# Performance work log

Measured on AMD Instinct MI355X. Metric: run time of the kernel, lower is better.

Reference implementation:

```python
import jax, jax.numpy as jnp
import numpy as np

H, D = 4, 32            # heads, head_dim
HID = H * D             # hidden_channels = 128
L = 2                   # num_layers
N = (100000, 50000)     # (n_session, n_item)
E = 200000              # edges per relation
ETYPES = ((0, 1), (1, 0), (1, 1))  # (src_type, dst_type) per relation


def _seg_softmax(alpha, dst, num_dst):
    # alpha: [E, H]; softmax over edges sharing the same dst node
    amax = jax.ops.segment_max(alpha, dst, num_segments=num_dst)
    amax = jnp.where(jnp.isfinite(amax), amax, 0.0)
    ex = jnp.exp(alpha - amax[dst])
    s = jax.ops.segment_sum(ex, dst, num_segments=num_dst)
    return ex / (s[dst] + 1e-16)


def _hgt_conv(xs, Wk, bk, Wq, bq, Wv, bv, Wa, ba, skip, a_rel, m_rel, p_rel, edges):
    # per-node-type k/q/v projections, reshaped to [N_t, H, D]
    k = [(x @ Wk[t] + bk[t]).reshape(-1, H, D) for t, x in enumerate(xs)]
    q = [(x @ Wq[t] + bq[t]).reshape(-1, H, D) for t, x in enumerate(xs)]
    v = [(x @ Wv[t] + bv[t]).reshape(-1, H, D) for t, x in enumerate(xs)]
    agg = [jnp.zeros((N[t], H, D), xs[0].dtype) for t in range(len(xs))]
    scale = 1.0 / jnp.sqrt(jnp.asarray(D, xs[0].dtype))
    for r, ((st, dt), (src, dst)) in enumerate(zip(ETYPES, edges)):
        kr = jnp.einsum('nhd,hde->nhe', k[st], a_rel[r])  # relation-specific key
        vr = jnp.einsum('nhd,hde->nhe', v[st], m_rel[r])  # relation-specific value
        alpha = jnp.einsum('ehd,ehd->eh', q[dt][dst], kr[src]) * p_rel[r] * scale
        alpha = _seg_softmax(alpha, dst, N[dt])
        msg = vr[src] * alpha[..., None]                  # [E, H, D]
        agg[dt] = agg[dt] + jax.ops.segment_sum(msg, dst, num_segments=N[dt])
    out = []
    for t in range(len(xs)):
        o = jax.nn.gelu(agg[t].reshape(N[t], HID), approximate=False) @ Wa[t] + ba[t]
        a = jax.nn.sigmoid(skip[t])
        out.append(a * o + (1.0 - a) * xs[t])
    return out


def setup_inputs() -> dict:
    key = jax.random.key(0)
    ks = jax.random.split(key, 16)
    f_in = 128
    s = 1.0 / np.sqrt(HID)
    return {
        'x0': jax.random.normal(ks[0], (N[0], f_in), jnp.float32),
        'x1': jax.random.normal(ks[1], (N[1], f_in), jnp.float32),
        'src0': jax.random.randint(ks[2], (E,), 0, N[0], jnp.int32),
        'dst0': jax.random.randint(ks[3], (E,), 0, N[1], jnp.int32),
        'src1': jax.random.randint(ks[4], (E,), 0, N[1], jnp.int32),
        'dst1': jax.random.randint(ks[5], (E,), 0, N[0], jnp.int32),
        'src2': jax.random.randint(ks[6], (E,), 0, N[1], jnp.int32),
        'dst2': jax.random.randint(ks[7], (E,), 0, N[1], jnp.int32),
        'W_in': jax.random.normal(ks[8], (2, f_in, HID), jnp.float32) / np.sqrt(f_in),
        'b_in': jnp.zeros((2, HID), jnp.float32),
        'Wk': jax.random.normal(ks[9], (L, 2, HID, HID), jnp.float32) * s,
        'bk': jnp.zeros((L, 2, HID), jnp.float32),
        'Wq': jax.random.normal(ks[10], (L, 2, HID, HID), jnp.float32) * s,
        'bq': jnp.zeros((L, 2, HID), jnp.float32),
        'Wv': jax.random.normal(ks[11], (L, 2, HID, HID), jnp.float32) * s,
        'bv': jnp.zeros((L, 2, HID), jnp.float32),
        'Wa': jax.random.normal(ks[12], (L, 2, HID, HID), jnp.float32) * s,
        'ba': jnp.zeros((L, 2, HID), jnp.float32),
        'skip': jnp.ones((L, 2), jnp.float32),
        'a_rel': jax.random.normal(ks[13], (L, 3, H, D, D), jnp.float32) / np.sqrt(D),
        'm_rel': jax.random.normal(ks[14], (L, 3, H, D, D), jnp.float32) / np.sqrt(D),
        'p_rel': jnp.ones((L, 3, H), jnp.float32),
    }


def reference(x0, x1, src0, dst0, src1, dst1, src2, dst2,
              W_in, b_in, Wk, bk, Wq, bq, Wv, bv, Wa, ba, skip,
              a_rel, m_rel, p_rel):
    edges = ((src0, dst0), (src1, dst1), (src2, dst2))
    h = [jax.nn.relu(x0 @ W_in[0] + b_in[0]),
         jax.nn.relu(x1 @ W_in[1] + b_in[1])]
    outs = [h]
    for l in range(L):
        h = _hgt_conv(h, Wk[l], bk[l], Wq[l], bq[l], Wv[l], bv[l],
                      Wa[l], ba[l], skip[l], a_rel[l], m_rel[l], p_rel[l], edges)
        outs.append(h)
    y0 = jnp.concatenate([o[0] for o in outs], axis=1)  # [N0, HID*(L+1)]
    y1 = jnp.concatenate([o[1] for o in outs], axis=1)  # [N1, HID*(L+1)]
    return (y0, y1)
```

## Files before the change

kernel.cpp:

```cpp
#include <hip/hip_runtime.h>
#include <math.h>


#define HID 128
#define OLD 384

typedef __attribute__((ext_vector_type(8))) short short8;
typedef __attribute__((ext_vector_type(4))) float f32x4;

__device__ __forceinline__ unsigned short f2b(float f) {
    unsigned u = __float_as_uint(f);
    u += 0x7fffu + ((u >> 16) & 1u);
    return (unsigned short)(u >> 16);
}
__device__ __forceinline__ unsigned pk2(float a, float b) {
    return (unsigned)f2b(a) | ((unsigned)f2b(b) << 16);
}
__device__ __forceinline__ float blo(unsigned u) { return __uint_as_float(u << 16); }
__device__ __forceinline__ float bhi(unsigned u) { return __uint_as_float(u & 0xffff0000u); }
__device__ __forceinline__ float gelu_f(float x) {
    return 0.5f * x * (1.0f + erff(x * 0.70710678118654752f));
}

__device__ __forceinline__ void nt_st_f32x4(float* p, float a, float b,
                                            float c, float d) {
    f32x4 v = {a, b, c, d};
    __builtin_nontemporal_store(v, (f32x4*)p);
}
__device__ __forceinline__ f32x4 nt_ld_f32x4(const float* p) {
    return __builtin_nontemporal_load((const f32x4*)p);
}

template <int AFP32>
__device__ __forceinline__ void load_bfrag(short8 (&d)[4], const void* Aptr,
                                           int lda, int node, int kq)
{
    if (AFP32) {
        const float* ar = (const float*)Aptr + (size_t)node * lda;
#pragma unroll
        for (int kt = 0; kt < 4; ++kt) {
            f32x4 v0 = nt_ld_f32x4(ar + kt * 32 + kq * 8);
            f32x4 v1 = nt_ld_f32x4(ar + kt * 32 + kq * 8 + 4);
            short8 t;
            t[0] = (short)f2b(v0[0]); t[1] = (short)f2b(v0[1]);
            t[2] = (short)f2b(v0[2]); t[3] = (short)f2b(v0[3]);
            t[4] = (short)f2b(v1[0]); t[5] = (short)f2b(v1[1]);
            t[6] = (short)f2b(v1[2]); t[7] = (short)f2b(v1[3]);
            d[kt] = t;
        }
    } else {
        const unsigned short* ar = (const unsigned short*)Aptr + (size_t)node * lda;
#pragma unroll
        for (int kt = 0; kt < 4; ++kt)
            d[kt] = *(const short8*)(ar + kt * 32 + kq * 8);
    }
}

template <int AFP32, int EPI, int BRES>
__device__ __forceinline__ void gemm_body(
    int yb,
    const void* __restrict__ A0, const void* __restrict__ A1, int lda,
    const unsigned short* __restrict__ Wp, const float* __restrict__ biasP,
    int wblk0, int wblk1, int nct0, int nct1,
    unsigned short* __restrict__ Cb0, unsigned short* __restrict__ Cb1,
    int ldcb0, int ldcb1,
    float* __restrict__ Cf0, float* __restrict__ Cf1, int ldcf,
    const unsigned short* __restrict__ Hb0, const unsigned short* __restrict__ Hb1,
    const float* __restrict__ skipP,
    int M0, int M1, int yb0)
{
    const int tid  = threadIdx.x;
    const int wid  = tid >> 6;
    const int lane = tid & 63;
    const int ow = (wid >> 1) * 64;
    const int nw = (wid & 1) * 64;
    const int lm = lane & 15;
    const int kq = lane >> 4;

    const int t  = (yb >= yb0) ? 1 : 0;
    const int r0 = (t ? (yb - yb0) : yb) * 128;
    const int M    = t ? M1 : M0;
    const int nct  = t ? nct1 : nct0;
    const int wblk = t ? wblk1 : wblk0;
    const void* Aptr = t ? A1 : A0;
    unsigned short* Cb = t ? Cb1 : Cb0;
    const int ldcb = t ? ldcb1 : ldcb0;
    float* Cf = t ? Cf1 : Cf0;
    const unsigned short* Hb = t ? Hb1 : Hb0;

    short8 bres[4][4];
    if (BRES) {
#pragma unroll
        for (int ni = 0; ni < 4; ++ni) {
            int node = r0 + nw + ni * 16 + lm;
            node = (node < M) ? node : (M - 1);
            load_bfrag<AFP32>(bres[ni], Aptr, lda, node, kq);
        }
    }

    float aa = 0.f, ab = 0.f;
    if (EPI == 2) {
        const float sv = skipP[t];
        aa = 1.0f / (1.0f + __expf(-sv));
        ab = 1.0f - aa;
    }

    for (int ct = 0; ct < nct; ++ct) {
        const unsigned short* wbase = Wp + (size_t)(wblk + ct) * 16384;
        short8 wf[4][4];
#pragma unroll
        for (int mi = 0; mi < 4; ++mi) {
            const int mt = (ow >> 4) + mi;
#pragma unroll
            for (int kt = 0; kt < 4; ++kt)
                wf[mi][kt] = *(const short8*)(wbase + (((mt * 4 + kt) * 64 + lane) << 3));
        }

        f32x4 acc[4][4];
#pragma unroll
        for (int ni = 0; ni < 4; ++ni)
#pragma unroll
            for (int mi = 0; mi < 4; ++mi)
                acc[ni][mi] = (f32x4){0.f, 0.f, 0.f, 0.f};

#pragma unroll
        for (int ni = 0; ni < 4; ++ni) {
            if (BRES) {
#pragma unroll
                for (int kt = 0; kt < 4; ++kt)
#pragma unroll
                    for (int mi = 0; mi < 4; ++mi)
                        acc[ni][mi] = __builtin_amdgcn_mfma_f32_16x16x32_bf16(
                            wf[mi][kt], bres[ni][kt], acc[ni][mi], 0, 0, 0);
            } else {
                int node = r0 + nw + ni * 16 + lm;
                node = (node < M) ? node : (M - 1);
                short8 bl[4];
                load_bfrag<AFP32>(bl, Aptr, lda, node, kq);
#pragma unroll
                for (int kt = 0; kt < 4; ++kt)
#pragma unroll
                    for (int mi = 0; mi < 4; ++mi)
                        acc[ni][mi] = __builtin_amdgcn_mfma_f32_16x16x32_bf16(
                            wf[mi][kt], bl[kt], acc[ni][mi], 0, 0, 0);
            }
        }

        float4 b4[4];
#pragma unroll
        for (int mi = 0; mi < 4; ++mi)
            b4[mi] = *(const float4*)(biasP + (wblk + ct) * 128 + ow + mi * 16 + kq * 4);

#pragma unroll
        for (int ni = 0; ni < 4; ++ni) {
            const int node = r0 + nw + ni * 16 + lm;
            if (node >= M) continue;
#pragma unroll
            for (int mi = 0; mi < 4; ++mi) {
                const int oc = ow + mi * 16 + kq * 4;
                float v0 = acc[ni][mi][0] + b4[mi].x;
                float v1 = acc[ni][mi][1] + b4[mi].y;
                float v2 = acc[ni][mi][2] + b4[mi].z;
                float v3 = acc[ni][mi][3] + b4[mi].w;
                if (EPI == 1) {
                    v0 = fmaxf(v0, 0.f); v1 = fmaxf(v1, 0.f);
                    v2 = fmaxf(v2, 0.f); v3 = fmaxf(v3, 0.f);
                }
                if (EPI == 2) {
                    uint2 hp = *(const uint2*)(Hb + (size_t)node * 128 + oc);
                    v0 = aa * v0 + ab * blo(hp.x);
                    v1 = aa * v1 + ab * bhi(hp.x);
                    v2 = aa * v2 + ab * blo(hp.y);
                    v3 = aa * v3 + ab * bhi(hp.y);
                }
                if (EPI != 0) {
                    nt_st_f32x4(Cf + (size_t)node * ldcf + oc, v0, v1, v2, v3);
                    *(uint2*)(Cb + (size_t)node * 128 + oc) =
                        make_uint2(pk2(v0, v1), pk2(v2, v3));
                } else {
                    *(uint2*)(Cb + (size_t)node * ldcb + ct * 128 + oc) =
                        make_uint2(pk2(v0, v1), pk2(v2, v3));
                }
            }
        }
    }
}

template <int AFP32, int EPI, int BRES>
__global__ __launch_bounds__(256) void mfma_gemm(
    const void* __restrict__ A0, const void* __restrict__ A1, int lda,
    const unsigned short* __restrict__ Wp, const float* __restrict__ biasP,
    int wblk0, int wblk1, int nct0, int nct1,
    unsigned short* __restrict__ Cb0, unsigned short* __restrict__ Cb1,
    int ldcb0, int ldcb1,
    float* __restrict__ Cf0, float* __restrict__ Cf1, int ldcf,
    const unsigned short* __restrict__ Hb0, const unsigned short* __restrict__ Hb1,
    const float* __restrict__ skipP,
    int M0, int M1, int yb0)
{
    gemm_body<AFP32, EPI, BRES>(blockIdx.x, A0, A1, lda, Wp, biasP,
        wblk0, wblk1, nct0, nct1, Cb0, Cb1, ldcb0, ldcb1,
        Cf0, Cf1, ldcf, Hb0, Hb1, skipP, M0, M1, yb0);
}

__device__ __forceinline__ void attn_loop4(
    const unsigned short* __restrict__ kv, int ldkv, int koff, int voff,
    const int* __restrict__ rowptr, const int* __restrict__ esrc,
    int n, int g, const float* qf,
    float* a, float& lO)
{
    const int p0 = rowptr[n], p1 = rowptr[n + 1];
    float m = -1e30f, l = 0.f;
#pragma unroll
    for (int j = 0; j < 8; ++j) a[j] = 0.f;
    if (p0 < p1) {
        const int nit = (p1 - p0 + 3) >> 2;
        int p = p0 + g;
        bool valid = (p < p1);
        {
            const int s = esrc[valid ? p : (p1 - 1)];
            const unsigned short* rp = kv + (size_t)s * ldkv;
            uint4 kp = *(const uint4*)(rp + koff);
            uint4 vp = *(const uint4*)(rp + voff);
            for (int it = 0; it < nit; ++it) {
                const uint4 kc = kp, vc = vp;
                const bool vld = valid;
                p += 4;
                if (it + 1 < nit) {
                    valid = (p < p1);
                    const int s2 = esrc[valid ? p : (p1 - 1)];
                    const unsigned short* r2 = kv + (size_t)s2 * ldkv;
                    kp = *(const uint4*)(r2 + koff);
                    vp = *(const uint4*)(r2 + voff);
                }
                float al = qf[0] * blo(kc.x) + qf[1] * bhi(kc.x);
                al += qf[2] * blo(kc.y) + qf[3] * bhi(kc.y);
                al += qf[4] * blo(kc.z) + qf[5] * bhi(kc.z);
                al += qf[6] * blo(kc.w) + qf[7] * bhi(kc.w);
                al += __shfl_xor(al, 1, 64);
                al += __shfl_xor(al, 2, 64);
                al = vld ? al : -2e30f;
                const float nm  = fmaxf(m, al);
                const float scl = __expf(m - nm);
                const float w   = __expf(al - nm);
                l = l * scl + w;
                a[0] = a[0] * scl + w * blo(vc.x);
                a[1] = a[1] * scl + w * bhi(vc.x);
                a[2] = a[2] * scl + w * blo(vc.y);
                a[3] = a[3] * scl + w * bhi(vc.y);
                a[4] = a[4] * scl + w * blo(vc.z);
                a[5] = a[5] * scl + w * bhi(vc.z);
                a[6] = a[6] * scl + w * blo(vc.w);
                a[7] = a[7] * scl + w * bhi(vc.w);
                m = nm;
            }
        }
    }
    float mo = fmaxf(m, __shfl_xor(m, 16, 64));
    const float M = fmaxf(mo, __shfl_xor(mo, 32, 64));
    const float sc = __expf(m - M);
    l *= sc;
#pragma unroll
    for (int j = 0; j < 8; ++j) a[j] *= sc;
    l += __shfl_xor(l, 16, 64);
    l += __shfl_xor(l, 32, 64);
#pragma unroll
    for (int j = 0; j < 8; ++j) {
        a[j] += __shfl_xor(a[j], 16, 64);
        a[j] += __shfl_xor(a[j], 32, 64);
    }
    lO = l;
}

__global__ __launch_bounds__(256) void hgt_attn(
    const unsigned short* __restrict__ qkv0,
    const unsigned short* __restrict__ qkv1,
    const int* __restrict__ rp1, const int* __restrict__ es1,
    const int* __restrict__ rp0, const int* __restrict__ es0,
    const int* __restrict__ rp2, const int* __restrict__ es2,
    unsigned short* __restrict__ agg0, unsigned short* __restrict__ agg1,
    int N0, int N1, int nb1)
{
    const int wid = threadIdx.x >> 6, lane = threadIdx.x & 63;
    const int u = lane & 15, g = lane >> 4;
    const int uo = u * 8;
    const int b = blockIdx.x;
    float qf[8];
    if (b < nb1) {
        const int n = b * 4 + wid;
        if (n >= N1) return;
        const uint4 qp = *(const uint4*)(qkv1 + (size_t)n * 640 + uo);
        qf[0] = blo(qp.x); qf[1] = bhi(qp.x);
        qf[2] = blo(qp.y); qf[3] = bhi(qp.y);
        qf[4] = blo(qp.z); qf[5] = bhi(qp.z);
        qf[6] = blo(qp.w); qf[7] = bhi(qp.w);
        float ax[8], ay[8], lx, ly;
        attn_loop4(qkv0, 384, 128 + uo, 256 + uo, rp0, es0, n, g, qf, ax, lx);
        attn_loop4(qkv1, 640, 384 + uo, 512 + uo, rp2, es2, n, g, qf, ay, ly);
        if (g == 0) {
            const float ix = 1.0f / (lx + 1e-16f);
            const float iy = 1.0f / (ly + 1e-16f);
            uint4 o;
            o.x = pk2(gelu_f(ax[0] * ix + ay[0] * iy), gelu_f(ax[1] * ix + ay[1] * iy));
            o.y = pk2(gelu_f(ax[2] * ix + ay[2] * iy), gelu_f(ax[3] * ix + ay[3] * iy));
            o.z = pk2(gelu_f(ax[4] * ix + ay[4] * iy), gelu_f(ax[5] * ix + ay[5] * iy));
            o.w = pk2(gelu_f(ax[6] * ix + ay[6] * iy), gelu_f(ax[7] * ix + ay[7] * iy));
            *(uint4*)(agg1 + (size_t)n * 128 + uo) = o;
        }
    } else {
        const int n = (b - nb1) * 4 + wid;
        if (n >= N0) return;
        const uint4 qp = *(const uint4*)(qkv0 + (size_t)n * 384 + uo);
        qf[0] = blo(qp.x); qf[1] = bhi(qp.x);
        qf[2] = blo(qp.y); qf[3] = bhi(qp.y);
        qf[4] = blo(qp.z); qf[5] = bhi(qp.z);
        qf[6] = blo(qp.w); qf[7] = bhi(qp.w);
        float av[8], lv;
        attn_loop4(qkv1, 640, 128 + uo, 256 + uo, rp1, es1, n, g, qf, av, lv);
        if (g == 0) {
            const float inv = 1.0f / (lv + 1e-16f);
            uint4 o;
            o.x = pk2(gelu_f(av[0] * inv), gelu_f(av[1] * inv));
            o.y = pk2(gelu_f(av[2] * inv), gelu_f(av[3] * inv));
            o.z = pk2(gelu_f(av[4] * inv), gelu_f(av[5] * inv));
            o.w = pk2(gelu_f(av[6] * inv), gelu_f(av[7] * inv));
            *(uint4*)(agg0 + (size_t)n * 128 + uo) = o;
        }
    }
}

__global__ void hgt_prep(
    const float* __restrict__ W_in, const float* __restrict__ b_in,
    const float* __restrict__ Wk, const float* __restrict__ bk,
    const float* __restrict__ Wq, const float* __restrict__ bq,
    const float* __restrict__ Wv, const float* __restrict__ bv,
    const float* __restrict__ Wa, const float* __restrict__ ba,
    const float* __restrict__ a_rel, const float* __restrict__ m_rel,
    const float* __restrict__ p_rel,
    unsigned short* __restrict__ Bp, float* __restrict__ bp,
    const int* __restrict__ d0, const int* __restrict__ d1,
    const int* __restrict__ d2, int E, int N0v, int N1v,
    int* __restrict__ deg)
{
    if (blockIdx.y < 3) {
        const int r = blockIdx.y;
        const int e = blockIdx.x * 256 + threadIdx.x;
        if (e >= E) return;
        const int* dd = (r == 0) ? d0 : (r == 1) ? d1 : d2;
        const int doff = (r == 0) ? 0 : (r == 1) ? N1v : (N1v + N0v);
        atomicAdd(&deg[doff + dd[e]], 1);
        return;
    }
    const int bid = blockIdx.x;
    if (bid >= 22) return;

    const float* Wsrc = nullptr;
    const float* bsrc = nullptr;
    int l = -1, r = 0, kv = 0;
    if      (bid <  2) { Wsrc = W_in + (size_t)bid * 16384; bsrc = b_in + bid * 128; }
    else if (bid == 2) { Wsrc = Wq;                bsrc = bq; }
    else if (bid <= 4) { l = 0; r = 0; kv = bid - 3; }
    else if (bid == 5) { Wsrc = Wq + 16384;        bsrc = bq + 128; }
    else if (bid <= 7) { l = 0; r = 1; kv = bid - 6; }
    else if (bid <= 9) { l = 0; r = 2; kv = bid - 8; }
    else if (bid == 10){ Wsrc = Wa;                bsrc = ba; }
    else if (bid == 11){ Wsrc = Wa + 16384;        bsrc = ba + 128; }
    else if (bid == 12){ Wsrc = Wq + 2 * 16384;    bsrc = bq + 256; }
    else if (bid <= 14){ l = 1; r = 0; kv = bid - 13; }
    else if (bid == 15){ Wsrc = Wq + 3 * 16384;    bsrc = bq + 384; }
    else if (bid <= 17){ l = 1; r = 1; kv = bid - 16; }
    else if (bid <= 19){ l = 1; r = 2; kv = bid - 18; }
    else if (bid == 20){ Wsrc = Wa + 2 * 16384;    bsrc = ba + 256; }
    else               { Wsrc = Wa + 3 * 16384;    bsrc = ba + 384; }

    const bool iscw = (l >= 0);
    const float* rel = nullptr;
    if (iscw) {
        const int st = (r == 0) ? 0 : 1;
        Wsrc = (kv ? Wv : Wk) + (size_t)(l * 2 + st) * 16384;
        bsrc = (kv ? bv : bk) + (l * 2 + st) * 128;
        rel  = (kv ? m_rel : a_rel) + (size_t)(l * 3 + r) * 4096;
    }

    for (int i = threadIdx.x; i < 16384; i += 256) {
        const int mt = i >> 11, kt = (i >> 9) & 3, ln = (i >> 3) & 63, j = i & 7;
        const int m = mt * 16 + (ln & 15);
        const int k = kt * 32 + (ln >> 4) * 8 + j;
        float v;
        if (!iscw) {
            v = Wsrc[k * 128 + m];
        } else {
            const int h = m >> 5, e = m & 31;
            const float fac = kv ? 1.0f
                : p_rel[(l * 3 + r) * 4 + h] * 0.17677669529663687f;
            const float* wr = Wsrc + (size_t)k * 128 + h * 32;
            const float* rc = rel + h * 1024 + e;
            float s = 0.f;
#pragma unroll
            for (int d = 0; d < 32; ++d) s = fmaf(wr[d], rc[d * 32], s);
            v = s * fac;
        }
        Bp[(size_t)bid * 16384 + i] = f2b(v);
    }
    if (threadIdx.x < 128) {
        const int n = threadIdx.x;
        float v;
        if (!iscw) {
            v = bsrc[n];
        } else {
            const int h = n >> 5, e = n & 31;
            const float fac = kv ? 1.0f
                : p_rel[(l * 3 + r) * 4 + h] * 0.17677669529663687f;
            const float* rc = rel + h * 1024 + e;
            float s = 0.f;
#pragma unroll
            for (int d = 0; d < 32; ++d) s = fmaf(bsrc[h * 32 + d], rc[d * 32], s);
            v = s * fac;
        }
        bp[bid * 128 + n] = v;
    }
}

__global__ void hgt_scan1(const int* __restrict__ deg, int* __restrict__ rowptr,
                          int* __restrict__ bsums, int N0v, int N1v)
{
    const int r = blockIdx.y;
    const int Nd = (r == 1) ? N0v : N1v;
    const int n  = Nd + 1;
    if (blockIdx.x * 512 >= n) return;
    const int doff = (r == 0) ? 0 : (r == 1) ? N1v : (N1v + N0v);
    const int roff = (r == 0) ? 0 : (r == 1) ? (N1v + 1) : (N1v + N0v + 2);
    __shared__ int s[512];
    const int tid = threadIdx.x;
    const int i = blockIdx.x * 512 + tid;
    const int v = (i < Nd) ? deg[doff + i] : 0;
    s[tid] = v;
    __syncthreads();
    for (int off = 1; off < 512; off <<= 1) {
        const int t = (tid >= off) ? s[tid - off] : 0;
        __syncthreads();
        s[tid] += t;
        __syncthreads();
    }
    if (i < n) rowptr[roff + i] = s[tid] - v;
    if (tid == 511) bsums[r * 256 + blockIdx.x] = s[511];
}

__global__ void hgt_scan23(int* __restrict__ rowptr, const int* __restrict__ bsums,
                           int N0v, int N1v)
{
    const int r = blockIdx.y;
    const int n = ((r == 1) ? N0v : N1v) + 1;
    if (blockIdx.x * 512 >= n) return;
    const int roff = (r == 0) ? 0 : (r == 1) ? (N1v + 1) : (N1v + N0v + 2);
    const int tid = threadIdx.x;
    int v = (tid < (int)blockIdx.x) ? bsums[r * 256 + tid] : 0;
#pragma unroll
    for (int o = 1; o < 64; o <<= 1) v += __shfl_xor(v, o, 64);
    __shared__ int ws[8];
    if ((tid & 63) == 0) ws[tid >> 6] = v;
    __syncthreads();
    int base = 0;
#pragma unroll
    for (int k = 0; k < 8; ++k) base += ws[k];
    const int i = blockIdx.x * 512 + tid;
    if (i < n) rowptr[roff + i] += base;
}

__global__ __launch_bounds__(256) void hgt_fill_inproj(
    const int* __restrict__ s0, const int* __restrict__ d0,
    const int* __restrict__ s1, const int* __restrict__ d1,
    const int* __restrict__ s2, const int* __restrict__ d2,
    int E, int N0v, int N1v,
    const int* __restrict__ rowptr, int* __restrict__ cnt,
    int* __restrict__ esrc, int eb,
    const float* __restrict__ x0, const float* __restrict__ x1,
    const unsigned short* __restrict__ Wp, const float* __restrict__ biasP,
    unsigned short* __restrict__ hb0, unsigned short* __restrict__ hb1,
    float* __restrict__ outp, int nGemm, int yb0)
{
    const int b = blockIdx.x;
    if (b < nGemm) {
        gemm_body<1, 1, 0>(b, x0, x1, 128, Wp, biasP, 0, 1, 1, 1,
                           hb0, hb1, 128, 128,
                           outp, outp + (size_t)N0v * OLD, OLD,
                           nullptr, nullptr, nullptr, N0v, N1v, yb0);
        return;
    }
    const int bb = b - nGemm;
    const int r = bb / eb;
    const int e = (bb - r * eb) * 256 + (int)threadIdx.x;
    if (e >= E) return;
    const int* ss = (r == 0) ? s0 : (r == 1) ? s1 : s2;
    const int* dd = (r == 0) ? d0 : (r == 1) ? d1 : d2;
    const int doff = (r == 0) ? 0 : (r == 1) ? N1v : (N1v + N0v);
    const int roff = (r == 0) ? 0 : (r == 1) ? (N1v + 1) : (N1v + N0v + 2);
    const int d = dd[e];
    const int pos = atomicAdd(&cnt[doff + d], 1);
    esrc[(size_t)r * E + rowptr[roff + d] + pos] = ss[e];
}

extern "C" void kernel_launch(void* const* d_in, const int* in_sizes, int n_in,
                              void* d_out, int out_size, void* d_ws, size_t ws_size,
                              hipStream_t stream)
{
    const float* x0  = (const float*)d_in[0];
    const float* x1  = (const float*)d_in[1];
    const int* src0 = (const int*)d_in[2];
    const int* dst0 = (const int*)d_in[3];
    const int* src1 = (const int*)d_in[4];
    const int* dst1 = (const int*)d_in[5];
    const int* src2 = (const int*)d_in[6];
    const int* dst2 = (const int*)d_in[7];
    const float* W_in = (const float*)d_in[8];
    const float* b_in = (const float*)d_in[9];
    const float* Wk = (const float*)d_in[10];
    const float* bk = (const float*)d_in[11];
    const float* Wq = (const float*)d_in[12];
    const float* bq = (const float*)d_in[13];
    const float* Wv = (const float*)d_in[14];
    const float* bv = (const float*)d_in[15];
    const float* Wa = (const float*)d_in[16];
    const float* ba = (const float*)d_in[17];
    const float* skip = (const float*)d_in[18];
    const float* a_rel = (const float*)d_in[19];
    const float* m_rel = (const float*)d_in[20];
    const float* p_rel = (const float*)d_in[21];

    const int N0 = in_sizes[0] / HID;
    const int N1 = in_sizes[1] / HID;
    const int E  = in_sizes[2];
    float* out = (float*)d_out;
    (void)n_in; (void)out_size; (void)ws_size;

    char* p = (char*)d_ws;
    auto carve = [&](size_t bytes) -> char* {
        char* q = p;
        p += (bytes + 255) & ~(size_t)255;
        return q;
    };
    unsigned short* hbf  = (unsigned short*)carve((size_t)(N0 + N1) * 128 * 2);
    unsigned short* qkv0 = (unsigned short*)carve((size_t)N0 * 384 * 2);
    unsigned short* qkv1 = (unsigned short*)carve((size_t)N1 * 640 * 2);
    unsigned short* agg  = (unsigned short*)carve((size_t)(N0 + N1) * 128 * 2);
    unsigned short* packW = (unsigned short*)carve((size_t)22 * 16384 * 2);
    float* packb = (float*)carve((size_t)22 * 128 * 4);
    int* rowptr = (int*)carve((size_t)(N0 + 2 * N1 + 3) * 4);
    int* esrc   = (int*)carve((size_t)3 * E * 4);
    char* zbase = carve(0);
    int* deg   = (int*)carve((size_t)(N0 + 2 * N1) * 4);
    int* cnt   = (int*)carve((size_t)(N0 + 2 * N1) * 4);
    int* bsums = (int*)carve(3 * 256 * 4);
    const size_t zbytes = (size_t)((char*)(bsums + 3 * 256) - zbase);

    unsigned short* hbf1 = hbf + (size_t)N0 * 128;
    unsigned short* agg0 = agg;
    unsigned short* agg1 = agg + (size_t)N0 * 128;
    const int* rp0 = rowptr;
    const int* rp1 = rowptr + (N1 + 1);
    const int* rp2 = rowptr + (N1 + N0 + 2);
    const int* es0 = esrc;
    const int* es1 = esrc + (size_t)E;
    const int* es2 = esrc + (size_t)2 * E;

    const int eb  = (E + 255) / 256;
    const int nbx = (N0 + 1 + 511) / 512;
    const int mbN0 = (N0 + 127) / 128;
    const int mbN1 = (N1 + 127) / 128;
    const int nGemm = mbN0 + mbN1;

    hipMemsetAsync(zbase, 0, zbytes, stream);

    hgt_prep<<<dim3(eb, 4), 256, 0, stream>>>(
        W_in, b_in, Wk, bk, Wq, bq, Wv, bv, Wa, ba,
        a_rel, m_rel, p_rel, packW, packb,
        dst0, dst1, dst2, E, N0, N1, deg);

    hgt_scan1 <<<dim3(nbx, 3), 512, 0, stream>>>(deg, rowptr, bsums, N0, N1);
    hgt_scan23<<<dim3(nbx, 3), 512, 0, stream>>>(rowptr, bsums, N0, N1);

    hgt_fill_inproj<<<nGemm + 3 * eb, 256, 0, stream>>>(
        src0, dst0, src1, dst1, src2, dst2, E, N0, N1,
        rowptr, cnt, (int*)esrc, eb,
        x0, x1, packW, packb, hbf, hbf1, out, nGemm, mbN0);

    for (int l = 0; l < 2; ++l) {
        const int qkv0_blk = l ? 12 : 2;
        const int qkv1_blk = l ? 15 : 5;
        const int out0_blk = l ? 20 : 10;
        const int out1_blk = l ? 21 : 11;

        mfma_gemm<0, 0, 1><<<nGemm, 256, 0, stream>>>(
            hbf1, hbf, 128, packW, packb,
            qkv1_blk, qkv0_blk, 5, 3,
            qkv1, qkv0, 640, 384,
            nullptr, nullptr, 0,
            nullptr, nullptr, nullptr,
            N1, N0, mbN1);

        const int nb1 = (N1 + 3) / 4;
        const int nb0 = (N0 + 3) / 4;
        hgt_attn<<<nb1 + nb0, 256, 0, stream>>>(
            qkv0, qkv1, rp1, es1, rp0, es0, rp2, es2,
            agg0, agg1, N0, N1, nb1);

        mfma_gemm<0, 2, 0><<<nGemm, 256, 0, stream>>>(
            agg0, agg1, 128, packW, packb,
            out0_blk, out1_blk, 1, 1,
            hbf, hbf1, 128, 128,
            out + (size_t)(l + 1) * 128,
            out + (size_t)N0 * OLD + (size_t)(l + 1) * 128, OLD,
            hbf, hbf1, skip + l * 2, N0, N1, mbN0);
    }
}
```

Before: 834.0 us.

## Fuse edge attention with output projection GEMM via LDS-staged tiles

The separate attention kernel and output-projection GEMM are merged into one kernel. Each block computes attention for 128 destination nodes, storing the GELU outputs as bf16 in a swizzled LDS tile. It then runs the MFMA output projection with the skip blend directly from LDS. This removes the agg intermediate buffer's global write and read plus one launch per layer. The cost is coarser parallelism: each wave now processes 32 nodes serially, and the 32KB LDS per block limits occupancy, which may reduce latency hiding for the irregular gathers.

Result: slower. 964.6 us (+15.7%).

```diff
diff --git a/kernel.cpp b/kernel.cpp
--- a/kernel.cpp
+++ b/kernel.cpp
@@ -65,8 +65,6 @@
     unsigned short* __restrict__ Cb0, unsigned short* __restrict__ Cb1,
     int ldcb0, int ldcb1,
     float* __restrict__ Cf0, float* __restrict__ Cf1, int ldcf,
-    const unsigned short* __restrict__ Hb0, const unsigned short* __restrict__ Hb1,
-    const float* __restrict__ skipP,
     int M0, int M1, int yb0)
 {
     const int tid  = threadIdx.x;
@@ -86,7 +84,6 @@
     unsigned short* Cb = t ? Cb1 : Cb0;
     const int ldcb = t ? ldcb1 : ldcb0;
     float* Cf = t ? Cf1 : Cf0;
-    const unsigned short* Hb = t ? Hb1 : Hb0;
 
     short8 bres[4][4];
     if (BRES) {
@@ -96,13 +93,6 @@
             node = (node < M) ? node : (M - 1);
             load_bfrag<AFP32>(bres[ni], Aptr, lda, node, kq);
         }
-    }
-
-    float aa = 0.f, ab = 0.f;
-    if (EPI == 2) {
-        const float sv = skipP[t];
-        aa = 1.0f / (1.0f + __expf(-sv));
-        ab = 1.0f - aa;
     }
 
     for (int ct = 0; ct < nct; ++ct) {
@@ -166,13 +156,6 @@
                     v0 = fmaxf(v0, 0.f); v1 = fmaxf(v1, 0.f);
                     v2 = fmaxf(v2, 0.f); v3 = fmaxf(v3, 0.f);
                 }
-                if (EPI == 2) {
-                    uint2 hp = *(const uint2*)(Hb + (size_t)node * 128 + oc);
-                    v0 = aa * v0 + ab * blo(hp.x);
-                    v1 = aa * v1 + ab * bhi(hp.x);
-                    v2 = aa * v2 + ab * blo(hp.y);
-                    v3 = aa * v3 + ab * bhi(hp.y);
-                }
                 if (EPI != 0) {
                     nt_st_f32x4(Cf + (size_t)node * ldcf + oc, v0, v1, v2, v3);
                     *(uint2*)(Cb + (size_t)node * 128 + oc) =
@@ -194,13 +177,11 @@
     unsigned short* __restrict__ Cb0, unsigned short* __restrict__ Cb1,
     int ldcb0, int ldcb1,
     float* __restrict__ Cf0, float* __restrict__ Cf1, int ldcf,
-    const unsigned short* __restrict__ Hb0, const unsigned short* __restrict__ Hb1,
-    const float* __restrict__ skipP,
     int M0, int M1, int yb0)
 {
     gemm_body<AFP32, EPI, BRES>(blockIdx.x, A0, A1, lda, Wp, biasP,
         wblk0, wblk1, nct0, nct1, Cb0, Cb1, ldcb0, ldcb1,
-        Cf0, Cf1, ldcf, Hb0, Hb1, skipP, M0, M1, yb0);
+        Cf0, Cf1, ldcf, M0, M1, yb0);
 }
 
 __device__ __forceinline__ void attn_loop4(
@@ -272,59 +253,140 @@
     lO = l;
 }
 
-__global__ __launch_bounds__(256) void hgt_attn(
+__global__ __launch_bounds__(256) void hgt_attn_outproj(
     const unsigned short* __restrict__ qkv0,
     const unsigned short* __restrict__ qkv1,
     const int* __restrict__ rp1, const int* __restrict__ es1,
     const int* __restrict__ rp0, const int* __restrict__ es0,
     const int* __restrict__ rp2, const int* __restrict__ es2,
-    unsigned short* __restrict__ agg0, unsigned short* __restrict__ agg1,
-    int N0, int N1, int nb1)
-{
-    const int wid = threadIdx.x >> 6, lane = threadIdx.x & 63;
+    const unsigned short* __restrict__ Wp, const float* __restrict__ biasP,
+    int wblk0, int wblk1,
+    unsigned short* __restrict__ hb0, unsigned short* __restrict__ hb1,
+    float* __restrict__ outp0, float* __restrict__ outp1, int ldcf,
+    const float* __restrict__ skipP,
+    int M0, int M1, int yb0)
+{
+    __shared__ __align__(16) unsigned short lds[128 * 128];
+    const int tid = threadIdx.x;
+    const int wid = tid >> 6, lane = tid & 63;
     const int u = lane & 15, g = lane >> 4;
     const int uo = u * 8;
     const int b = blockIdx.x;
-    float qf[8];
-    if (b < nb1) {
-        const int n = b * 4 + wid;
-        if (n >= N1) return;
-        const uint4 qp = *(const uint4*)(qkv1 + (size_t)n * 640 + uo);
-        qf[0] = blo(qp.x); qf[1] = bhi(qp.x);
-        qf[2] = blo(qp.y); qf[3] = bhi(qp.y);
-        qf[4] = blo(qp.z); qf[5] = bhi(qp.z);
-        qf[6] = blo(qp.w); qf[7] = bhi(qp.w);
-        float ax[8], ay[8], lx, ly;
-        attn_loop4(qkv0, 384, 128 + uo, 256 + uo, rp0, es0, n, g, qf, ax, lx);
-        attn_loop4(qkv1, 640, 384 + uo, 512 + uo, rp2, es2, n, g, qf, ay, ly);
-        if (g == 0) {
-            const float ix = 1.0f / (lx + 1e-16f);
-            const float iy = 1.0f / (ly + 1e-16f);
-            uint4 o;
-            o.x = pk2(gelu_f(ax[0] * ix + ay[0] * iy), gelu_f(ax[1] * ix + ay[1] * iy));
-            o.y = pk2(gelu_f(ax[2] * ix + ay[2] * iy), gelu_f(ax[3] * ix + ay[3] * iy));
-            o.z = pk2(gelu_f(ax[4] * ix + ay[4] * iy), gelu_f(ax[5] * ix + ay[5] * iy));
-            o.w = pk2(gelu_f(ax[6] * ix + ay[6] * iy), gelu_f(ax[7] * ix + ay[7] * iy));
-            *(uint4*)(agg1 + (size_t)n * 128 + uo) = o;
-        }
-    } else {
-        const int n = (b - nb1) * 4 + wid;
-        if (n >= N0) return;
-        const uint4 qp = *(const uint4*)(qkv0 + (size_t)n * 384 + uo);
-        qf[0] = blo(qp.x); qf[1] = bhi(qp.x);
-        qf[2] = blo(qp.y); qf[3] = bhi(qp.y);
-        qf[4] = blo(qp.z); qf[5] = bhi(qp.z);
-        qf[6] = blo(qp.w); qf[7] = bhi(qp.w);
-        float av[8], lv;
-        attn_loop4(qkv1, 640, 128 + uo, 256 + uo, rp1, es1, n, g, qf, av, lv);
-        if (g == 0) {
-            const float inv = 1.0f / (lv + 1e-16f);
-            uint4 o;
-            o.x = pk2(gelu_f(av[0] * inv), gelu_f(av[1] * inv));
-            o.y = pk2(gelu_f(av[2] * inv), gelu_f(av[3] * inv));
-            o.z = pk2(gelu_f(av[4] * inv), gelu_f(av[5] * inv));
-            o.w = pk2(gelu_f(av[6] * inv), gelu_f(av[7] * inv));
-            *(uint4*)(agg0 + (size_t)n * 128 + uo) = o;
+    const int is1 = (b < yb0) ? 1 : 0;
+    const int r0 = (is1 ? b : (b - yb0)) * 128;
+    const int M  = is1 ? M1 : M0;
+
+    for (int j = 0; j < 32; ++j) {
+        const int local = wid * 32 + j;
+        const int n = r0 + local;
+        if (n < M) {
+            float o[8];
+            if (is1) {
+                const uint4 qp = *(const uint4*)(qkv1 + (size_t)n * 640 + uo);
+                float qf[8];
+                qf[0] = blo(qp.x); qf[1] = bhi(qp.x);
+                qf[2] = blo(qp.y); qf[3] = bhi(qp.y);
+                qf[4] = blo(qp.z); qf[5] = bhi(qp.z);
+                qf[6] = blo(qp.w); qf[7] = bhi(qp.w);
+                float ax[8], ay[8], lx, ly;
+                attn_loop4(qkv0, 384, 128 + uo, 256 + uo, rp0, es0, n, g, qf, ax, lx);
+                attn_loop4(qkv1, 640, 384 + uo, 512 + uo, rp2, es2, n, g, qf, ay, ly);
+                const float ix = 1.0f / (lx + 1e-16f);
+                const float iy = 1.0f / (ly + 1e-16f);
+#pragma unroll
+                for (int k = 0; k < 8; ++k) o[k] = gelu_f(ax[k] * ix + ay[k] * iy);
+            } else {
+                const uint4 qp = *(const uint4*)(qkv0 + (size_t)n * 384 + uo);
+                float qf[8];
+                qf[0] = blo(qp.x); qf[1] = bhi(qp.x);
+                qf[2] = blo(qp.y); qf[3] = bhi(qp.y);
+                qf[4] = blo(qp.z); qf[5] = bhi(qp.z);
+                qf[6] = blo(qp.w); qf[7] = bhi(qp.w);
+                float av[8], lv;
+                attn_loop4(qkv1, 640, 128 + uo, 256 + uo, rp1, es1, n, g, qf, av, lv);
+                const float inv = 1.0f / (lv + 1e-16f);
+#pragma unroll
+                for (int k = 0; k < 8; ++k) o[k] = gelu_f(av[k] * inv);
+            }
+            if (g == 0) {
+                const int byte = local * 256 + ((u * 16) ^ ((local & 7) << 4));
+                *(uint4*)((char*)lds + byte) =
+                    make_uint4(pk2(o[0], o[1]), pk2(o[2], o[3]),
+                               pk2(o[4], o[5]), pk2(o[6], o[7]));
+            }
+        }
+    }
+    __syncthreads();
+
+    const int ow = (wid >> 1) * 64;
+    const int nw = (wid & 1) * 64;
+    const int lm = lane & 15;
+    const int kq = lane >> 4;
+    const int wblk = is1 ? wblk1 : wblk0;
+    unsigned short* Hb = is1 ? hb1 : hb0;
+    float* Cf = is1 ? outp1 : outp0;
+    const float sv = skipP[is1];
+    const float aa = 1.0f / (1.0f + __expf(-sv));
+    const float ab = 1.0f - aa;
+
+    short8 wf[4][4];
+    const unsigned short* wbase = Wp + (size_t)wblk * 16384;
+#pragma unroll
+    for (int mi = 0; mi < 4; ++mi) {
+        const int mt = (ow >> 4) + mi;
+#pragma unroll
+        for (int kt = 0; kt < 4; ++kt)
+            wf[mi][kt] = *(const short8*)(wbase + (((mt * 4 + kt) * 64 + lane) << 3));
+    }
+
+    f32x4 acc[4][4];
+#pragma unroll
+    for (int ni = 0; ni < 4; ++ni)
+#pragma unroll
+        for (int mi = 0; mi < 4; ++mi)
+            acc[ni][mi] = (f32x4){0.f, 0.f, 0.f, 0.f};
+
+#pragma unroll
+    for (int ni = 0; ni < 4; ++ni) {
+        const int local = nw + ni * 16 + lm;
+        short8 bl[4];
+#pragma unroll
+        for (int kt = 0; kt < 4; ++kt) {
+            const int byte = local * 256 + ((kt * 64 + kq * 16) ^ ((local & 7) << 4));
+            bl[kt] = *(const short8*)((const char*)lds + byte);
+        }
+#pragma unroll
+        for (int kt = 0; kt < 4; ++kt)
+#pragma unroll
+            for (int mi = 0; mi < 4; ++mi)
+                acc[ni][mi] = __builtin_amdgcn_mfma_f32_16x16x32_bf16(
+                    wf[mi][kt], bl[kt], acc[ni][mi], 0, 0, 0);
+    }
+
+    float4 b4[4];
+#pragma unroll
+    for (int mi = 0; mi < 4; ++mi)
+        b4[mi] = *(const float4*)(biasP + wblk * 128 + ow + mi * 16 + kq * 4);
+
+#pragma unroll
+    for (int ni = 0; ni < 4; ++ni) {
+        const int node = r0 + nw + ni * 16 + lm;
+        if (node >= M) continue;
+#pragma unroll
+        for (int mi = 0; mi < 4; ++mi) {
+            const int oc = ow + mi * 16 + kq * 4;
+            float v0 = acc[ni][mi][0] + b4[mi].x;
+            float v1 = acc[ni][mi][1] + b4[mi].y;
+            float v2 = acc[ni][mi][2] + b4[mi].z;
+            float v3 = acc[ni][mi][3] + b4[mi].w;
+            uint2 hp = *(const uint2*)(Hb + (size_t)node * 128 + oc);
+            v0 = aa * v0 + ab * blo(hp.x);
+            v1 = aa * v1 + ab * bhi(hp.x);
+            v2 = aa * v2 + ab * blo(hp.y);
+            v3 = aa * v3 + ab * bhi(hp.y);
+            nt_st_f32x4(Cf + (size_t)node * ldcf + oc, v0, v1, v2, v3);
+            *(uint2*)(Hb + (size_t)node * 128 + oc) =
+                make_uint2(pk2(v0, v1), pk2(v2, v3));
         }
     }
 }
@@ -484,7 +546,7 @@
         gemm_body<1, 1, 0>(b, x0, x1, 128, Wp, biasP, 0, 1, 1, 1,
                            hb0, hb1, 128, 128,
                            outp, outp + (size_t)N0v * OLD, OLD,
-                           nullptr, nullptr, nullptr, N0v, N1v, yb0);
+                           N0v, N1v, yb0);
         return;
     }
     const int bb = b - nGemm;
@@ -542,7 +604,6 @@
     unsigned short* hbf  = (unsigned short*)carve((size_t)(N0 + N1) * 128 * 2);
     unsigned short* qkv0 = (unsigned short*)carve((size_t)N0 * 384 * 2);
     unsigned short* qkv1 = (unsigned short*)carve((size_t)N1 * 640 * 2);
-    unsigned short* agg  = (unsigned short*)carve((size_t)(N0 + N1) * 128 * 2);
     unsigned short* packW = (unsigned short*)carve((size_t)22 * 16384 * 2);
     float* packb = (float*)carve((size_t)22 * 128 * 4);
     int* rowptr = (int*)carve((size_t)(N0 + 2 * N1 + 3) * 4);
@@ -554,8 +615,6 @@
     const size_t zbytes = (size_t)((char*)(bsums + 3 * 256) - zbase);
 
     unsigned short* hbf1 = hbf + (size_t)N0 * 128;
-    unsigned short* agg0 = agg;
-    unsigned short* agg1 = agg + (size_t)N0 * 128;
     const int* rp0 = rowptr;
     const int* rp1 = rowptr + (N1 + 1);
     const int* rp2 = rowptr + (N1 + N0 + 2);
@@ -595,21 +654,14 @@
             qkv1_blk, qkv0_blk, 5, 3,
             qkv1, qkv0, 640, 384,
             nullptr, nullptr, 0,
-            nullptr, nullptr, nullptr,
             N1, N0, mbN1);
 
-        const int nb1 = (N1 + 3) / 4;
-        const int nb0 = (N0 + 3) / 4;
-        hgt_attn<<<nb1 + nb0, 256, 0, stream>>>(
+        hgt_attn_outproj<<<mbN1 + mbN0, 256, 0, stream>>>(
             qkv0, qkv1, rp1, es1, rp0, es0, rp2, es2,
-            agg0, agg1, N0, N1, nb1);
-
-        mfma_gemm<0, 2, 0><<<nGemm, 256, 0, stream>>>(
-            agg0, agg1, 128, packW, packb,
-            out0_blk, out1_blk, 1, 1,
-            hbf, hbf1, 128, 128,
+            packW, packb, out0_blk, out1_blk,
+            hbf, hbf1,
             out + (size_t)(l + 1) * 128,
             out + (size_t)N0 * OLD + (size_t)(l + 1) * 128, OLD,
-            hbf, hbf1, skip + l * 2, N0, N1, mbN0);
-    }
-}
+            skip + l * 2, N0, N1, mbN1);
+    }
+}
```
